# Kernel optimization log

Hardware: AMD Instinct MI355X
Metric: run time of the kernel (lower is better)

## Reference

```python
import jax, jax.numpy as jnp
import numpy as np


def setup_inputs() -> dict:
    key = jax.random.key(0)
    # coeffs_tensor: stacked/padded wavelet coefficients [B, F, T]
    coeffs = jax.random.normal(key, (16, 256, 8192), dtype=jnp.float32)
    return {"coeffs": coeffs}


def reference(coeffs) -> jnp.ndarray:
    B, F, T = coeffs.shape
    # torch.angle on a real tensor -> 0 for x>=0, pi for x<0; jnp.angle matches.
    phase = jnp.angle(coeffs)
    inst_freq = jnp.diff(phase, axis=-1)
    inst_freq = jnp.pad(inst_freq, ((0, 0), (0, 0), (0, 1)))  # F.pad(..., (0,1))
    freq_adjusted = jnp.clip(inst_freq, -1.0, 1.0)  # [B,F,T]
    # k = (f + freq_adjusted).long(); .long() truncates toward zero, as does astype(int32)
    f_idx = jnp.arange(F, dtype=coeffs.dtype)[None, :, None]
    k = jnp.clip((f_idx + freq_adjusted).astype(jnp.int32), 0, F - 1)  # [B,F,T]
    # Fused scatter-add over all (b, f, t): sst[b, k[b,f,t], t] += coeffs[b, f, t]
    b_idx = jnp.arange(B)[:, None, None]
    t_idx = jnp.arange(T)[None, None, :]
    sst = jnp.zeros_like(coeffs).at[b_idx, k, t_idx].add(coeffs)
    return sst
```

## Files before the change

### kernel.cpp

```cpp
#include <hip/hip_runtime.h>

#define BB 16
#define FF 256
#define TT 8192
#define F_CHUNK 16
#define THREADS 256

__device__ __forceinline__ int sgn_bit(float x) {
    return (int)(__float_as_uint(x) >> 31);
}

struct Raw { float4 v; float e; };

__global__ __launch_bounds__(THREADS) void sst_kernel(const float* __restrict__ in,
                                                      float* __restrict__ out) {
    const int t    = blockIdx.x * (THREADS * 4) + threadIdx.x * 4;
    const int fs   = blockIdx.y * F_CHUNK;
    const int b    = blockIdx.z;
    const int lane = threadIdx.x & 63;

    const float* src = in  + (size_t)b * FF * TT + t;
    float*       dst = out + (size_t)b * FF * TT + t;

    const bool tail = (t + 4 >= TT);

    auto load_raw = [&](int f) {
        Raw r;
        r.v = *reinterpret_cast<const float4*>(src + (size_t)f * TT);
        r.e = (lane == 63 && !tail) ? src[(size_t)f * TT + 4] : 0.0f;
        return r;
    };
    auto adj_of = [&](const Raw& r) {
        float nxt = __shfl_down(r.v.x, 1, 64);
        if (lane == 63) nxt = r.e;
        const int s0 = sgn_bit(r.v.x), s1 = sgn_bit(r.v.y), s2 = sgn_bit(r.v.z),
                  s3 = sgn_bit(r.v.w), s4 = sgn_bit(nxt);
        int4 a;
        a.x = s1 - s0;
        a.y = s2 - s1;
        a.z = s3 - s2;
        a.w = tail ? 0 : (s4 - s3);
        return a;
    };

    float4 vprev, vcur, vnext;
    int4   aprev, acur, anext;
    Raw    rn, rn2;

    if (fs == 0) {
        aprev = make_int4(9, 9, 9, 9);
        vprev = make_float4(0.f, 0.f, 0.f, 0.f);
    } else {
        Raw r = load_raw(fs - 1);
        vprev = r.v; aprev = adj_of(r);
    }
    {
        Raw r = load_raw(fs);
        vcur = r.v; acur = adj_of(r);
    }
    rn = load_raw(fs + 1);

    #pragma unroll
    for (int i = 0; i < F_CHUNK; ++i) {
        const int g = fs + i;

        const bool want2 = (i + 2 <= F_CHUNK) && (g + 2 < FF);
        if (want2) rn2 = load_raw(g + 2);

        if (g + 1 < FF) {
            vnext = rn.v; anext = adj_of(rn);
        } else {
            anext = make_int4(9, 9, 9, 9);
            vnext = make_float4(0.f, 0.f, 0.f, 0.f);
        }

        const bool isFirst = (g == 0);
        const bool isLast  = (g == FF - 1);

        float4 r;
        {
            const bool bc = (acur.x == 0) || (isFirst && acur.x < 0) || (isLast && acur.x > 0);
            r.x = ((aprev.x == 1) ? vprev.x : 0.f) + (bc ? vcur.x : 0.f)
                + ((anext.x == -1) ? vnext.x : 0.f);
        }
        {
            const bool bc = (acur.y == 0) || (isFirst && acur.y < 0) || (isLast && acur.y > 0);
            r.y = ((aprev.y == 1) ? vprev.y : 0.f) + (bc ? vcur.y : 0.f)
                + ((anext.y == -1) ? vnext.y : 0.f);
        }
        {
            const bool bc = (acur.z == 0) || (isFirst && acur.z < 0) || (isLast && acur.z > 0);
            r.z = ((aprev.z == 1) ? vprev.z : 0.f) + (bc ? vcur.z : 0.f)
                + ((anext.z == -1) ? vnext.z : 0.f);
        }
        {
            const bool bc = (acur.w == 0) || (isFirst && acur.w < 0) || (isLast && acur.w > 0);
            r.w = ((aprev.w == 1) ? vprev.w : 0.f) + (bc ? vcur.w : 0.f)
                + ((anext.w == -1) ? vnext.w : 0.f);
        }

        *reinterpret_cast<float4*>(dst + (size_t)g * TT) = r;

        vprev = vcur;  aprev = acur;
        vcur  = vnext; acur  = anext;
        rn    = rn2;
    }
}

extern "C" void kernel_launch(void* const* d_in, const int* in_sizes, int n_in,
                              void* d_out, int out_size, void* d_ws, size_t ws_size,
                              hipStream_t stream) {
    const float* in  = (const float*)d_in[0];
    float*       out = (float*)d_out;
    dim3 grid(TT / (THREADS * 4), FF / F_CHUNK, BB);
    sst_kernel<<<grid, THREADS, 0, stream>>>(in, out);
}
```

Baseline: 241.2 us.

## Load all rows upfront, drop cross-lane shuffle, pack sign deltas in bits

Each thread now issues every load for its F-chunk (halved to 8, plus two halo rows) up front. It fetches the neighbour element with a per-thread scalar load instead of a wave shuffle plus lane-63 special case, and packs the per-element sign differences into a 2-bit field word. The aim is more memory-level parallelism and fewer instructions, with occupancy hinted via launch bounds. The cost is more halo reads, since two extra rows are read per 8 instead of per 16, plus redundant scalar loads that should mostly hit cache.

```diff
diff --git a/kernel.cpp b/kernel.cpp
--- a/kernel.cpp
+++ b/kernel.cpp
@@ -3,107 +3,86 @@
 #define BB 16
 #define FF 256
 #define TT 8192
-#define F_CHUNK 16
+#define F_CHUNK 8
+#define ROWS (F_CHUNK + 2)
 #define THREADS 256
 
 __device__ __forceinline__ int sgn_bit(float x) {
     return (int)(__float_as_uint(x) >> 31);
 }
 
-struct Raw { float4 v; float e; };
-
-__global__ __launch_bounds__(THREADS) void sst_kernel(const float* __restrict__ in,
-                                                      float* __restrict__ out) {
-    const int t    = blockIdx.x * (THREADS * 4) + threadIdx.x * 4;
-    const int fs   = blockIdx.y * F_CHUNK;
-    const int b    = blockIdx.z;
-    const int lane = threadIdx.x & 63;
+__global__ __launch_bounds__(THREADS, 8) void sst_kernel(const float* __restrict__ in,
+                                                         float* __restrict__ out) {
+    const int t  = blockIdx.x * (THREADS * 4) + threadIdx.x * 4;
+    const int fs = blockIdx.y * F_CHUNK;
+    const int b  = blockIdx.z;
 
     const float* src = in  + (size_t)b * FF * TT + t;
     float*       dst = out + (size_t)b * FF * TT + t;
 
     const bool tail = (t + 4 >= TT);
+    const int  eoff = tail ? 3 : 4;
 
-    auto load_raw = [&](int f) {
-        Raw r;
-        r.v = *reinterpret_cast<const float4*>(src + (size_t)f * TT);
-        r.e = (lane == 63 && !tail) ? src[(size_t)f * TT + 4] : 0.0f;
-        return r;
-    };
-    auto adj_of = [&](const Raw& r) {
-        float nxt = __shfl_down(r.v.x, 1, 64);
-        if (lane == 63) nxt = r.e;
-        const int s0 = sgn_bit(r.v.x), s1 = sgn_bit(r.v.y), s2 = sgn_bit(r.v.z),
-                  s3 = sgn_bit(r.v.w), s4 = sgn_bit(nxt);
-        int4 a;
-        a.x = s1 - s0;
-        a.y = s2 - s1;
-        a.z = s3 - s2;
-        a.w = tail ? 0 : (s4 - s3);
-        return a;
-    };
-
-    float4 vprev, vcur, vnext;
-    int4   aprev, acur, anext;
-    Raw    rn, rn2;
-
-    if (fs == 0) {
-        aprev = make_int4(9, 9, 9, 9);
-        vprev = make_float4(0.f, 0.f, 0.f, 0.f);
-    } else {
-        Raw r = load_raw(fs - 1);
-        vprev = r.v; aprev = adj_of(r);
-    }
-    {
-        Raw r = load_raw(fs);
-        vcur = r.v; acur = adj_of(r);
-    }
-    rn = load_raw(fs + 1);
+    float4   v[ROWS];
+    float    e[ROWS];
+    unsigned pk[ROWS];
 
     #pragma unroll
-    for (int i = 0; i < F_CHUNK; ++i) {
-        const int g = fs + i;
+    for (int i = 0; i < ROWS; ++i) {
+        const int f = fs - 1 + i;
+        if (f >= 0 && f < FF) {
+            const float* p = src + (size_t)f * TT;
+            v[i] = *reinterpret_cast<const float4*>(p);
+            e[i] = p[eoff];
+        } else {
+            v[i] = make_float4(0.f, 0.f, 0.f, 0.f);
+            e[i] = 0.f;
+        }
+    }
 
-        const bool want2 = (i + 2 <= F_CHUNK) && (g + 2 < FF);
-        if (want2) rn2 = load_raw(g + 2);
+    #pragma unroll
+    for (int i = 0; i < ROWS; ++i) {
+        const int s0 = sgn_bit(v[i].x), s1 = sgn_bit(v[i].y),
+                  s2 = sgn_bit(v[i].z), s3 = sgn_bit(v[i].w), s4 = sgn_bit(e[i]);
+        const int a0 = s1 - s0 + 1;
+        const int a1 = s2 - s1 + 1;
+        const int a2 = s3 - s2 + 1;
+        const int a3 = tail ? 1 : (s4 - s3 + 1);
+        pk[i] = (unsigned)(a0 | (a1 << 2) | (a2 << 4) | (a3 << 6));
+    }
 
-        if (g + 1 < FF) {
-            vnext = rn.v; anext = adj_of(rn);
-        } else {
-            anext = make_int4(9, 9, 9, 9);
-            vnext = make_float4(0.f, 0.f, 0.f, 0.f);
-        }
-
+    #pragma unroll
+    for (int i = 1; i <= F_CHUNK; ++i) {
+        const int g = fs + (i - 1);
         const bool isFirst = (g == 0);
         const bool isLast  = (g == FF - 1);
 
+        const unsigned pp = pk[i - 1], pc = pk[i], pn = pk[i + 1];
+        const float4   vp = v[i - 1],  vc = v[i],  vn = v[i + 1];
+
         float4 r;
         {
-            const bool bc = (acur.x == 0) || (isFirst && acur.x < 0) || (isLast && acur.x > 0);
-            r.x = ((aprev.x == 1) ? vprev.x : 0.f) + (bc ? vcur.x : 0.f)
-                + ((anext.x == -1) ? vnext.x : 0.f);
+            const unsigned cp = pp & 3u, cc = pc & 3u, cn = pn & 3u;
+            const bool bc = (cc == 1u) || (isFirst && cc == 0u) || (isLast && cc == 2u);
+            r.x = ((cp == 2u) ? vp.x : 0.f) + (bc ? vc.x : 0.f) + ((cn == 0u) ? vn.x : 0.f);
         }
         {
-            const bool bc = (acur.y == 0) || (isFirst && acur.y < 0) || (isLast && acur.y > 0);
-            r.y = ((aprev.y == 1) ? vprev.y : 0.f) + (bc ? vcur.y : 0.f)
-                + ((anext.y == -1) ? vnext.y : 0.f);
+            const unsigned cp = (pp >> 2) & 3u, cc = (pc >> 2) & 3u, cn = (pn >> 2) & 3u;
+            const bool bc = (cc == 1u) || (isFirst && cc == 0u) || (isLast && cc == 2u);
+            r.y = ((cp == 2u) ? vp.y : 0.f) + (bc ? vc.y : 0.f) + ((cn == 0u) ? vn.y : 0.f);
         }
         {
-            const bool bc = (acur.z == 0) || (isFirst && acur.z < 0) || (isLast && acur.z > 0);
-            r.z = ((aprev.z == 1) ? vprev.z : 0.f) + (bc ? vcur.z : 0.f)
-                + ((anext.z == -1) ? vnext.z : 0.f);
+            const unsigned cp = (pp >> 4) & 3u, cc = (pc >> 4) & 3u, cn = (pn >> 4) & 3u;
+            const bool bc = (cc == 1u) || (isFirst && cc == 0u) || (isLast && cc == 2u);
+            r.z = ((cp == 2u) ? vp.z : 0.f) + (bc ? vc.z : 0.f) + ((cn == 0u) ? vn.z : 0.f);
         }
         {
-            const bool bc = (acur.w == 0) || (isFirst && acur.w < 0) || (isLast && acur.w > 0);
-            r.w = ((aprev.w == 1) ? vprev.w : 0.f) + (bc ? vcur.w : 0.f)
-                + ((anext.w == -1) ? vnext.w : 0.f);
+            const unsigned cp = (pp >> 6) & 3u, cc = (pc >> 6) & 3u, cn = (pn >> 6) & 3u;
+            const bool bc = (cc == 1u) || (isFirst && cc == 0u) || (isLast && cc == 2u);
+            r.w = ((cp == 2u) ? vp.w : 0.f) + (bc ? vc.w : 0.f) + ((cn == 0u) ? vn.w : 0.f);
         }
 
         *reinterpret_cast<float4*>(dst + (size_t)g * TT) = r;
-
-        vprev = vcur;  aprev = acur;
-        vcur  = vnext; acur  = anext;
-        rn    = rn2;
     }
 }
 
```

Measured after the change: 240.6 us. Within noise of the previous version (-0.3%).
